# Kernel optimization log

Hardware: AMD Instinct MI355X
Metric: run time of the kernel (lower is better)

## Reference

```python
import jax, jax.numpy as jnp
import numpy as np

ALPHA = 100.0  # self.softmax_alpha


def _interp_nearest(x, size):
    # torch F.interpolate mode='nearest': src_idx = floor(dst_idx * H_in / H_out)
    H, W = x.shape[-2], x.shape[-1]
    h, w = size
    ri = (jnp.arange(h) * H) // h
    ci = (jnp.arange(w) * W) // w
    return x[:, :, ri, :][:, :, :, ci]


def _interp_bilinear_ac(x, size):
    # torch F.interpolate mode='bilinear', align_corners=True
    H, W = x.shape[-2], x.shape[-1]
    h, w = size

    def coords(n_out, n_in):
        if n_out == 1:
            return jnp.zeros((1,), jnp.float32)
        return jnp.arange(n_out, dtype=jnp.float32) * ((n_in - 1) / (n_out - 1))

    ry, rx = coords(h, H), coords(w, W)
    y0 = jnp.floor(ry).astype(jnp.int32)
    x0 = jnp.floor(rx).astype(jnp.int32)
    y1 = jnp.clip(y0 + 1, 0, H - 1)
    x1 = jnp.clip(x0 + 1, 0, W - 1)
    wy = (ry - y0.astype(jnp.float32))[None, None, :, None]
    wx = (rx - x0.astype(jnp.float32))[None, None, None, :]
    rows = x[:, :, y0, :] * (1.0 - wy) + x[:, :, y1, :] * wy  # (n,c,h,W)
    return rows[:, :, :, x0] * (1.0 - wx) + rows[:, :, :, x1] * wx  # (n,c,h,w)


def _warp(unalign_fb, fa, fa_parse, fb, fb_parse, alpha):
    n, c, h, w = fa.shape
    c2 = unalign_fb.shape[1]
    hw = h * w
    # center and channel-normalize features per spatial location
    fa = fa - jnp.mean(fa, axis=(2, 3), keepdims=True)
    fb = fb - jnp.mean(fb, axis=(2, 3), keepdims=True)
    fa = fa.reshape(n, c, hw)
    fb = fb.reshape(n, c, hw)
    fa = fa / jnp.linalg.norm(fa, axis=1, keepdims=True)
    fb = fb / jnp.linalg.norm(fb, axis=1, keepdims=True)
    ufb = unalign_fb.reshape(n, c2, hw)
    mask_a = (fa_parse.reshape(n, -1, hw)[:, 1:, :] != 0).astype(fa.dtype)  # (n,K,hw)
    mask_b = (fb_parse.reshape(n, -1, hw)[:, 1:, :] != 0).astype(fb.dtype)
    local_fa = fa[:, None, :, :] * mask_a[:, :, None, :]  # (n,K,c,hw)
    local_fb = fb[:, None, :, :] * mask_b[:, :, None, :]  # (n,K,c,hw)
    # energy[n,k,q,p] = sum_c local_fb[n,k,c,q] * local_fa[n,k,c,p]
    energy = jnp.einsum('nkcq,nkcp->nkqp', local_fb, local_fa) * alpha
    corr = jax.nn.softmax(energy, axis=2)  # softmax over fb locations q
    warped = jnp.einsum('ncq,nkqp->nkcp', ufb, corr)  # (n,K,c2,hw)
    combined = (warped * mask_a[:, :, None, :]).sum(axis=1)  # (n,c2,hw)
    norm = jnp.maximum(mask_a.sum(axis=1, keepdims=True), 1.0)  # (n,1,hw)
    aligned = combined / norm
    return aligned.reshape(n, c2, h, w)


def setup_inputs() -> dict:
    key = jax.random.key(0)
    k1, k2, k3, k4, k5 = jax.random.split(key, 5)
    return {
        'unalign_fb': jax.random.normal(k1, (1, 64, 256, 256), jnp.float32),
        'fa': jax.random.normal(k2, (1, 256, 64, 64), jnp.float32),
        'fa_parse': jax.random.randint(k3, (1, 4, 256, 256), 0, 2).astype(jnp.int32),
        'fb': jax.random.normal(k4, (1, 256, 64, 64), jnp.float32),
        'fb_parse': jax.random.randint(k5, (1, 4, 256, 256), 0, 2).astype(jnp.int32),
    }


def reference(unalign_fb, fa, fa_parse, fb, fb_parse):
    raw_hw = unalign_fb.shape[-2:]
    feat_hw = fa.shape[-2:]
    fa_p = _interp_nearest(fa_parse, feat_hw)
    fb_p = _interp_nearest(fb_parse, feat_hw)
    ufb = _interp_bilinear_ac(unalign_fb, fb.shape[-2:])
    aligned = _warp(ufb, fa, fa_p, fb, fb_p, ALPHA)
    return _interp_bilinear_ac(aligned, raw_hw)
```

## Files before the change

kernel.cpp:

```cpp
#include <hip/hip_runtime.h>
#include <math.h>

#define HW 4096
#define CC 256
#define C2 64
#define E50f 1.928749848e-22f

typedef unsigned short USH;
typedef __attribute__((ext_vector_type(8))) _Float16 f16x8;
typedef __attribute__((ext_vector_type(8))) short bf8;
typedef __attribute__((ext_vector_type(4))) float f32x4;

__device__ __forceinline__ USH f2bf(float x) {
    unsigned u = __float_as_uint(x);
    u += 0x7fff + ((u >> 16) & 1);
    return (USH)(u >> 16);
}
__device__ __forceinline__ USH f2h(float x) {
    _Float16 h = (_Float16)x;
    return *(USH*)&h;
}

__device__ __forceinline__ void gl2lds16(const USH* g, USH* l) {
    __builtin_amdgcn_global_load_lds(
        (const __attribute__((address_space(1))) void*)g,
        (__attribute__((address_space(3))) void*)l, 16, 0, 0);
}

__device__ __forceinline__ float block_reduce_sum_256(float v, float* sbuf) {
    int t = threadIdx.x;
    sbuf[t] = v;
    __syncthreads();
    for (int s = 128; s > 0; s >>= 1) {
        if (t < s) sbuf[t] += sbuf[t + s];
        __syncthreads();
    }
    float r = sbuf[0];
    __syncthreads();
    return r;
}

__global__ void k_channel_mean(const float* __restrict__ fa, const float* __restrict__ fb,
                               float* __restrict__ mu) {
    __shared__ float sbuf[256];
    int b = blockIdx.x;
    const float* src = (b < CC) ? (fa + b * HW) : (fb + (b - CC) * HW);
    float s = 0.f;
    for (int q = threadIdx.x; q < HW; q += 256) s += src[q];
    float tot = block_reduce_sum_256(s, sbuf);
    if (threadIdx.x == 0) mu[b] = tot * (1.0f / HW);
}

__global__ void k_norm_ss(const float* __restrict__ fa, const float* __restrict__ fb,
                          const float* __restrict__ mu, float* __restrict__ ssq_part) {
    int which = blockIdx.z;
    const float* src = which ? fb : fa;
    int p = blockIdx.x * 256 + threadIdx.x;
    int c0 = blockIdx.y * 32;
    float ss = 0.f;
    for (int c = c0; c < c0 + 32; ++c) {
        float v = src[c * HW + p] - mu[which * CC + c];
        ss += v * v;
    }
    ssq_part[(which * 8 + blockIdx.y) * HW + p] = ss;
}

__global__ __launch_bounds__(256) void k_norm_split_t(
    const float* __restrict__ fa, const float* __restrict__ fb,
    const float* __restrict__ mu, const float* __restrict__ ssq_part,
    USH* __restrict__ faT, USH* __restrict__ fbT) {
    __shared__ float tile[64][68];
    int which = blockIdx.z;
    const float* src = which ? fb : fa;
    USH* dst = which ? fbT : faT;
    int p0 = blockIdx.x * 64;
    int c0 = blockIdx.y * 64;
    int t = threadIdx.x;
    {
        int c_r = t >> 2, seg = t & 3;
        const float* s = &src[(size_t)(c0 + c_r) * HW + p0 + seg * 16];
#pragma unroll
        for (int k = 0; k < 4; ++k)
            *(float4*)&tile[c_r][seg * 16 + k * 4] = *(const float4*)&s[k * 4];
    }
    __syncthreads();
    {
        int p_r = t >> 2, seg = t & 3;
        int cl = seg * 16;
        float ss = 0.f;
#pragma unroll
        for (int z = 0; z < 8; ++z) ss += ssq_part[(which * 8 + z) * HW + p0 + p_r];
        float rinv = rsqrtf(ss);
        union { USH us[8]; uint4 v; } h0, h1;
#pragma unroll
        for (int j = 0; j < 8; ++j)
            h0.us[j] = f2h((tile[cl + j][p_r] - mu[which * CC + c0 + cl + j]) * rinv);
#pragma unroll
        for (int j = 0; j < 8; ++j)
            h1.us[j] = f2h((tile[cl + 8 + j][p_r] - mu[which * CC + c0 + cl + 8 + j]) * rinv);
        int kc = (c0 >> 5) + (seg >> 1);
        size_t base = (size_t)kc * 131072 + (size_t)(p0 + p_r) * 32 + (seg & 1) * 16;
        *(uint4*)&dst[base] = h0.v;
        *(uint4*)&dst[base + 8] = h1.v;
    }
}

__global__ void k_bilin_down_vt(const float* __restrict__ src, const int* __restrict__ fb_parse,
                                USH* __restrict__ vtT, float* __restrict__ bgbuf) {
    __shared__ float4 sbuf[256];
    int t = threadIdx.x;
    int p = blockIdx.x * 256 + t;
    int c = blockIdx.y;
    int j = p >> 6, i = p & 63;
    int off = (4 * j) * 256 + 4 * i;
    float m0 = (fb_parse[1 * 65536 + off] != 0) ? 1.f : 0.f;
    float m1 = (fb_parse[2 * 65536 + off] != 0) ? 1.f : 0.f;
    float m2 = (fb_parse[3 * 65536 + off] != 0) ? 1.f : 0.f;
    float ry = j * (255.0f / 63.0f);
    int y0 = (int)ry; y0 = min(y0, 255); int y1 = min(y0 + 1, 255);
    float wy = ry - (float)y0;
    float rx = i * (255.0f / 63.0f);
    int x0 = (int)rx; x0 = min(x0, 255); int x1 = min(x0 + 1, 255);
    float wx = rx - (float)x0;
    const float* sc = src + c * 65536;
    float r0 = sc[y0 * 256 + x0] * (1.f - wx) + sc[y0 * 256 + x1] * wx;
    float r1 = sc[y1 * 256 + x0] * (1.f - wx) + sc[y1 * 256 + x1] * wx;
    float v = r0 * (1.f - wy) + r1 * wy;
    size_t cbase = (size_t)(p >> 5) * 8192 + (p & 31);
    vtT[cbase + (0 * 65 + c) * 32] = f2bf(v * m0);
    vtT[cbase + (1 * 65 + c) * 32] = f2bf(v * m1);
    vtT[cbase + (2 * 65 + c) * 32] = f2bf(v * m2);
    if (c == 0) {
        vtT[cbase + 64 * 32]  = f2bf(m0);
        vtT[cbase + 129 * 32] = f2bf(m1);
        vtT[cbase + 194 * 32] = f2bf(m2);
        for (int m = 195; m < 256; ++m) vtT[cbase + m * 32] = 0;
    }
    float4 acc = make_float4(v, v * m0, v * m1, v * m2);
    sbuf[t] = acc;
    __syncthreads();
    for (int s = 128; s > 0; s >>= 1) {
        if (t < s) {
            float4 o = sbuf[t + s];
            sbuf[t].x += o.x; sbuf[t].y += o.y; sbuf[t].z += o.z; sbuf[t].w += o.w;
        }
        __syncthreads();
    }
    if (t == 0) {
        float4 r = sbuf[0];
        atomicAdd(&bgbuf[256 + c], r.x);
        atomicAdd(&bgbuf[0 * 65 + c], r.y);
        atomicAdd(&bgbuf[1 * 65 + c], r.z);
        atomicAdd(&bgbuf[2 * 65 + c], r.w);
    }
    __syncthreads();
    if (c == 0) {
        sbuf[t] = make_float4(m0, m1, m2, 0.f);
        __syncthreads();
        for (int s = 128; s > 0; s >>= 1) {
            if (t < s) {
                float4 o = sbuf[t + s];
                sbuf[t].x += o.x; sbuf[t].y += o.y; sbuf[t].z += o.z;
            }
            __syncthreads();
        }
        if (t == 0) {
            float4 r = sbuf[0];
            atomicAdd(&bgbuf[64], r.x);
            atomicAdd(&bgbuf[129], r.y);
            atomicAdd(&bgbuf[194], r.z);
        }
    }
}

__global__ __launch_bounds__(256) void k_gemm_s_exp(
    const USH* __restrict__ faT, const USH* __restrict__ fbT,
    USH* __restrict__ E) {
    __shared__ union { USH stage[2][2][4096]; USH ET[128][136]; } sm;
    int t = threadIdx.x;
    int qbase = blockIdx.x * 128;
    int pbase = blockIdx.y * 128;
    int w = t >> 6, lane = t & 63, lr = lane & 15, quad = lane >> 4;
    int pw = (w & 1) * 64, qw = (w >> 1) * 64;
    f32x4 acc[4][4] = {};

    const USH* srcA = faT + (size_t)pbase * 32;
    const USH* srcB = fbT + (size_t)qbase * 32;

#define STAGE_G(buf, kt)                                                        \
    {                                                                           \
        size_t ko = (size_t)(kt) * 131072;                                      \
        _Pragma("unroll")                                                       \
        for (int c = 0; c < 2; ++c) {                                           \
            int go = w * 1024 + c * 512 + lane * 8;                             \
            int lo = w * 1024 + c * 512;                                        \
            gl2lds16(srcA + ko + go, &sm.stage[buf][0][lo]);                    \
            gl2lds16(srcB + ko + go, &sm.stage[buf][1][lo]);                    \
        }                                                                       \
    }

    STAGE_G(0, 0);
    __syncthreads();
    for (int kt = 0; kt < 8; ++kt) {
        int cur = kt & 1;
        if (kt + 1 < 8) STAGE_G(cur ^ 1, kt + 1);
        f16x8 a[4], b[4];
#pragma unroll
        for (int i = 0; i < 4; ++i)
            a[i] = *(const f16x8*)&sm.stage[cur][0][(pw + 16 * i + lr) * 32 + quad * 8];
#pragma unroll
        for (int j = 0; j < 4; ++j)
            b[j] = *(const f16x8*)&sm.stage[cur][1][(qw + 16 * j + lr) * 32 + quad * 8];
#pragma unroll
        for (int i = 0; i < 4; ++i)
#pragma unroll
            for (int j = 0; j < 4; ++j)
                acc[i][j] = __builtin_amdgcn_mfma_f32_16x16x32_f16(a[i], b[j], acc[i][j], 0, 0, 0);
        __syncthreads();
    }
#undef STAGE_G
#pragma unroll
    for (int i = 0; i < 4; ++i) {
        int prow = pw + 16 * i + quad * 4;
#pragma unroll
        for (int j = 0; j < 4; ++j) {
            int qcol = qw + 16 * j + lr;
#pragma unroll
            for (int r = 0; r < 4; ++r)
                sm.ET[prow + r][qcol] = f2bf(__expf(fmaf(100.f, acc[i][j][r], -50.f)));
        }
    }
    __syncthreads();
    {
        int prow = t >> 1, half = t & 1;
#pragma unroll
        for (int cc = 0; cc < 2; ++cc) {
            int qcl = half * 2 + cc;
            size_t dst = (size_t)((qbase >> 5) + qcl) * 131072 + (size_t)(pbase + prow) * 32;
#pragma unroll
            for (int u = 0; u < 4; ++u)
                *(uint4*)&E[dst + u * 8] = *(const uint4*)&sm.ET[prow][qcl * 32 + u * 8];
        }
    }
}

__global__ __launch_bounds__(256) void k_pv(
    const USH* __restrict__ vtT, const USH* __restrict__ E,
    float* __restrict__ part) {
    __shared__ USH stage[2][2][4096];
    int t = threadIdx.x;
    int pbase = blockIdx.x * 128;
    int mbase = blockIdx.y * 128;
    int z = blockIdx.z;
    int w = t >> 6, lane = t & 63, lr = lane & 15, quad = lane >> 4;
    int mw = (w & 1) * 64, pw = (w >> 1) * 64;
    f32x4 acc[4][4] = {};

    const USH* srcA = vtT + (size_t)mbase * 32;
    const USH* srcB = E + (size_t)pbase * 32;

#define STAGE_P(buf, kt)                                                        \
    {                                                                           \
        size_t koA = (size_t)(z * 16 + (kt)) * 8192;                            \
        size_t koB = (size_t)(z * 16 + (kt)) * 131072;                          \
        _Pragma("unroll")                                                       \
        for (int c = 0; c < 2; ++c) {                                           \
            int go = w * 1024 + c * 512 + lane * 8;                             \
            int lo = w * 1024 + c * 512;                                        \
            gl2lds16(srcA + koA + go, &stage[buf][0][lo]);                      \
            gl2lds16(srcB + koB + go, &stage[buf][1][lo]);                      \
        }                                                                       \
    }

    STAGE_P(0, 0);
    __syncthreads();
    for (int kt = 0; kt < 16; ++kt) {
        int cur = kt & 1;
        if (kt + 1 < 16) STAGE_P(cur ^ 1, kt + 1);
        bf8 a[4], b[4];
#pragma unroll
        for (int i = 0; i < 4; ++i)
            a[i] = *(const bf8*)&stage[cur][0][(mw + 16 * i + lr) * 32 + quad * 8];
#pragma unroll
        for (int j = 0; j < 4; ++j)
            b[j] = *(const bf8*)&stage[cur][1][(pw + 16 * j + lr) * 32 + quad * 8];
#pragma unroll
        for (int i = 0; i < 4; ++i)
#pragma unroll
            for (int j = 0; j < 4; ++j)
                acc[i][j] = __builtin_amdgcn_mfma_f32_16x16x32_bf16(a[i], b[j], acc[i][j], 0, 0, 0);
        __syncthreads();
    }
#undef STAGE_P
    float* op = part + (size_t)z * 1048576;
#pragma unroll
    for (int i = 0; i < 4; ++i) {
        int mrow = mbase + mw + 16 * i + quad * 4;
#pragma unroll
        for (int j = 0; j < 4; ++j) {
            int pcol = pbase + pw + 16 * j + lr;
#pragma unroll
            for (int r = 0; r < 4; ++r)
                op[(size_t)(mrow + r) * HW + pcol] = acc[i][j][r];
        }
    }
}

__global__ void k_combine8(const float* __restrict__ part, const float* __restrict__ bgbuf,
                           const int* __restrict__ fa_parse, float* __restrict__ aligned) {
    int p = blockIdx.x * 256 + threadIdx.x;
    int c2 = blockIdx.y;
    int jj = p >> 6, ii = p & 63;
    int off = (4 * jj) * 256 + 4 * ii;
    float tot_c = bgbuf[256 + c2];
    float num = 0.f, s = 0.f;
    for (int k = 0; k < 3; ++k) {
        float ma = (fa_parse[(k + 1) * 65536 + off] != 0) ? 1.f : 0.f;
        s += ma;
        float den = E50f * (4096.0f - bgbuf[k * 65 + 64]);
        float nu  = E50f * (tot_c - bgbuf[k * 65 + c2]);
        size_t rd = (size_t)(k * 65 + 64) * HW + p;
        size_t rn = (size_t)(k * 65 + c2) * HW + p;
#pragma unroll
        for (int z = 0; z < 8; ++z) {
            den += part[(size_t)z * 1048576 + rd];
            nu  += part[(size_t)z * 1048576 + rn];
        }
        num += ma * (nu / den);
    }
    aligned[c2 * HW + p] = num / fmaxf(s, 1.f);
}

__global__ void k_bilin_up(const float* __restrict__ aligned, float* __restrict__ out) {
    int idx = (blockIdx.x * 256 + threadIdx.x) * 4;
    int c2 = blockIdx.y;
    int y = idx >> 8;
    float ry = y * (63.0f / 255.0f);
    int y0 = (int)ry; y0 = min(y0, 63); int y1 = min(y0 + 1, 63);
    float wy = ry - (float)y0;
    const float* a = aligned + c2 * HW;
    float4 o;
    float* op = &o.x;
#pragma unroll
    for (int u = 0; u < 4; ++u) {
        int x = (idx & 255) + u;
        float rx = x * (63.0f / 255.0f);
        int x0 = (int)rx; x0 = min(x0, 63); int x1 = min(x0 + 1, 63);
        float wx = rx - (float)x0;
        float r0 = a[y0 * 64 + x0] * (1.f - wx) + a[y0 * 64 + x1] * wx;
        float r1 = a[y1 * 64 + x0] * (1.f - wx) + a[y1 * 64 + x1] * wx;
        op[u] = r0 * (1.f - wy) + r1 * wy;
    }
    *(float4*)&out[c2 * 65536 + idx] = o;
}

extern "C" void kernel_launch(void* const* d_in, const int* in_sizes, int n_in,
                              void* d_out, int out_size, void* d_ws, size_t ws_size,
                              hipStream_t stream) {
    const float* unalign_fb = (const float*)d_in[0];
    const float* fa         = (const float*)d_in[1];
    const int*   fa_parse   = (const int*)d_in[2];
    const float* fb         = (const float*)d_in[3];
    const int*   fb_parse   = (const int*)d_in[4];
    float* out = (float*)d_out;

    float* w = (float*)d_ws;
    float* mu       = w;
    float* ssq_part = w + 512;
    float* bgbuf    = w + 66048;
    float* part     = w + 66368;
    float* aligned  = w + 8454976;
    USH* faT  = (USH*)(w + 8717120);
    USH* fbT  = (USH*)(w + 9241408);
    USH* vtT  = (USH*)(w + 9765696);
    USH* Ebuf = (USH*)(w + 10289984);

    k_channel_mean<<<dim3(512), dim3(256), 0, stream>>>(fa, fb, mu);
    k_norm_ss<<<dim3(16, 8, 2), dim3(256), 0, stream>>>(fa, fb, mu, ssq_part);
    k_norm_split_t<<<dim3(64, 4, 2), dim3(256), 0, stream>>>(fa, fb, mu, ssq_part, faT, fbT);
    hipMemsetAsync(bgbuf, 0, 320 * sizeof(float), stream);
    k_bilin_down_vt<<<dim3(16, 64), dim3(256), 0, stream>>>(unalign_fb, fb_parse, vtT, bgbuf);

    k_gemm_s_exp<<<dim3(32, 32), dim3(256), 0, stream>>>(faT, fbT, Ebuf);
    k_pv<<<dim3(32, 2, 8), dim3(256), 0, stream>>>(vtT, Ebuf, part);

    k_combine8<<<dim3(16, 64), dim3(256), 0, stream>>>(part, bgbuf, fa_parse, aligned);
    k_bilin_up<<<dim3(64, 64), dim3(256), 0, stream>>>(aligned, out);
}
```

Before: 150.7 us.

## Fuse QK-exp and PV GEMMs into flash-style attention kernel; merge prep kernels

Replaces the separate score+exp GEMM (which wrote a 4096x4096 bf16 E matrix to global memory) and the PV GEMM with one fused kernel that computes a 64-column score tile, exponentiates into LDS, and immediately multiplies by V, splitting q across 8 z-slices. The channel-mean and bilinear-downsample kernels are merged into one launch, and atomic reductions with a memset are replaced by per-block partial sums reduced in the combine kernel. This removes the large E round trip and several launches, at the cost of smaller tiles, fewer blocks (512), and more LDS per block.

```diff
diff --git a/kernel.cpp b/kernel.cpp
--- a/kernel.cpp
+++ b/kernel.cpp
@@ -27,28 +27,88 @@
         (__attribute__((address_space(3))) void*)l, 16, 0, 0);
 }
 
-__device__ __forceinline__ float block_reduce_sum_256(float v, float* sbuf) {
+__global__ void k_prep1(const float* __restrict__ fa, const float* __restrict__ fb,
+                        float* __restrict__ mu,
+                        const float* __restrict__ ufb_src, const int* __restrict__ fb_parse,
+                        USH* __restrict__ vtT, float* __restrict__ bgp) {
+    __shared__ float4 sred[256];
     int t = threadIdx.x;
-    sbuf[t] = v;
-    __syncthreads();
-    for (int s = 128; s > 0; s >>= 1) {
-        if (t < s) sbuf[t] += sbuf[t + s];
+    if (blockIdx.x < 512) {
+        int b = blockIdx.x;
+        const float* src = (b < CC) ? (fa + b * HW) : (fb + (b - CC) * HW);
+        float s = 0.f;
+        for (int q = t; q < HW; q += 256) s += src[q];
+        sred[t].x = s;
         __syncthreads();
-    }
-    float r = sbuf[0];
-    __syncthreads();
-    return r;
-}
-
-__global__ void k_channel_mean(const float* __restrict__ fa, const float* __restrict__ fb,
-                               float* __restrict__ mu) {
-    __shared__ float sbuf[256];
-    int b = blockIdx.x;
-    const float* src = (b < CC) ? (fa + b * HW) : (fb + (b - CC) * HW);
-    float s = 0.f;
-    for (int q = threadIdx.x; q < HW; q += 256) s += src[q];
-    float tot = block_reduce_sum_256(s, sbuf);
-    if (threadIdx.x == 0) mu[b] = tot * (1.0f / HW);
+        for (int st = 128; st > 0; st >>= 1) {
+            if (t < st) sred[t].x += sred[t + st].x;
+            __syncthreads();
+        }
+        if (t == 0) mu[b] = sred[0].x * (1.0f / HW);
+        return;
+    }
+    int bid = blockIdx.x - 512;
+    int pblk = bid & 15, c = bid >> 4;
+    int p = pblk * 256 + t;
+    int j = p >> 6, i = p & 63;
+    int off = (4 * j) * 256 + 4 * i;
+    float m0 = (fb_parse[1 * 65536 + off] != 0) ? 1.f : 0.f;
+    float m1 = (fb_parse[2 * 65536 + off] != 0) ? 1.f : 0.f;
+    float m2 = (fb_parse[3 * 65536 + off] != 0) ? 1.f : 0.f;
+    float ry = j * (255.0f / 63.0f);
+    int y0 = (int)ry; y0 = min(y0, 255); int y1 = min(y0 + 1, 255);
+    float wy = ry - (float)y0;
+    float rx = i * (255.0f / 63.0f);
+    int x0 = (int)rx; x0 = min(x0, 255); int x1 = min(x0 + 1, 255);
+    float wx = rx - (float)x0;
+    const float* sc = ufb_src + c * 65536;
+    float r0 = sc[y0 * 256 + x0] * (1.f - wx) + sc[y0 * 256 + x1] * wx;
+    float r1 = sc[y1 * 256 + x0] * (1.f - wx) + sc[y1 * 256 + x1] * wx;
+    float v = r0 * (1.f - wy) + r1 * wy;
+    size_t cbase = (size_t)(p >> 5) * 8192 + (p & 31);
+    vtT[cbase + (0 * 65 + c) * 32] = f2bf(v * m0);
+    vtT[cbase + (1 * 65 + c) * 32] = f2bf(v * m1);
+    vtT[cbase + (2 * 65 + c) * 32] = f2bf(v * m2);
+    if (c == 0) {
+        vtT[cbase + 64 * 32]  = f2bf(m0);
+        vtT[cbase + 129 * 32] = f2bf(m1);
+        vtT[cbase + 194 * 32] = f2bf(m2);
+        for (int m = 195; m < 256; ++m) vtT[cbase + m * 32] = 0;
+    }
+    sred[t] = make_float4(v, v * m0, v * m1, v * m2);
+    __syncthreads();
+    for (int st = 128; st > 0; st >>= 1) {
+        if (t < st) {
+            float4 o = sred[t + st];
+            sred[t].x += o.x; sred[t].y += o.y; sred[t].z += o.z; sred[t].w += o.w;
+        }
+        __syncthreads();
+    }
+    if (t == 0) {
+        float4 r = sred[0];
+        bgp[pblk * 320 + 256 + c]     = r.x;
+        bgp[pblk * 320 + 0 * 65 + c]  = r.y;
+        bgp[pblk * 320 + 1 * 65 + c]  = r.z;
+        bgp[pblk * 320 + 2 * 65 + c]  = r.w;
+    }
+    __syncthreads();
+    if (c == 0) {
+        sred[t] = make_float4(m0, m1, m2, 0.f);
+        __syncthreads();
+        for (int st = 128; st > 0; st >>= 1) {
+            if (t < st) {
+                float4 o = sred[t + st];
+                sred[t].x += o.x; sred[t].y += o.y; sred[t].z += o.z;
+            }
+            __syncthreads();
+        }
+        if (t == 0) {
+            float4 r = sred[0];
+            bgp[pblk * 320 + 64]  = r.x;
+            bgp[pblk * 320 + 129] = r.y;
+            bgp[pblk * 320 + 194] = r.z;
+        }
+    }
 }
 
 __global__ void k_norm_ss(const float* __restrict__ fa, const float* __restrict__ fb,
@@ -105,220 +165,131 @@
     }
 }
 
-__global__ void k_bilin_down_vt(const float* __restrict__ src, const int* __restrict__ fb_parse,
-                                USH* __restrict__ vtT, float* __restrict__ bgbuf) {
-    __shared__ float4 sbuf[256];
+__global__ __launch_bounds__(256, 2) void k_attn(
+    const USH* __restrict__ faT, const USH* __restrict__ fbT,
+    const USH* __restrict__ vtT, float* __restrict__ part) {
+    __shared__ USH sA[2][2048];
+    __shared__ USH sB[2][4096];
+    __shared__ USH sV[2][8192];
+    __shared__ USH sE[64 * 136];
     int t = threadIdx.x;
+    int p0 = blockIdx.x * 64;
+    int z = blockIdx.y;
+    int w = t >> 6, lane = t & 63, lr = lane & 15, quad = lane >> 4;
+    f32x4 accp[4][4] = {};
+
+    const USH* gA = faT + (size_t)p0 * 32;
+
+#define DMA_AB(buf, kc, q0)                                                          \
+    do {                                                                             \
+        gl2lds16(gA + (size_t)(kc) * 131072 + w * 512 + lane * 8, &sA[buf][w * 512]);\
+        _Pragma("unroll")                                                            \
+        for (int cc = 0; cc < 2; ++cc)                                               \
+            gl2lds16(fbT + (size_t)(kc) * 131072 + (size_t)(q0) * 32 +               \
+                         (2 * w + cc) * 512 + lane * 8,                              \
+                     &sB[buf][(2 * w + cc) * 512]);                                  \
+    } while (0)
+#define DMA_V(buf, qc)                                                               \
+    do {                                                                             \
+        _Pragma("unroll")                                                            \
+        for (int cc = 0; cc < 4; ++cc)                                               \
+            gl2lds16(vtT + (size_t)(qc) * 8192 + (4 * w + cc) * 512 + lane * 8,      \
+                     &sV[buf][(4 * w + cc) * 512]);                                  \
+    } while (0)
+
+    DMA_AB(0, 0, z * 512);
+    __syncthreads();
+    for (int qt = 0; qt < 4; ++qt) {
+        int q0 = z * 512 + qt * 128;
+        f32x4 accs[2][4] = {};
+        for (int kc = 0; kc < 8; ++kc) {
+            int cur = kc & 1;
+            if (kc < 7) DMA_AB(cur ^ 1, kc + 1, q0);
+            else        DMA_V(0, z * 16 + qt * 4);
+            f16x8 a[2], b[4];
+#pragma unroll
+            for (int i = 0; i < 2; ++i)
+                a[i] = *(const f16x8*)&sB[cur][(32 * w + 16 * i + lr) * 32 + quad * 8];
+#pragma unroll
+            for (int jj = 0; jj < 4; ++jj)
+                b[jj] = *(const f16x8*)&sA[cur][(16 * jj + lr) * 32 + quad * 8];
+#pragma unroll
+            for (int i = 0; i < 2; ++i)
+#pragma unroll
+                for (int jj = 0; jj < 4; ++jj)
+                    accs[i][jj] = __builtin_amdgcn_mfma_f32_16x16x32_f16(a[i], b[jj], accs[i][jj], 0, 0, 0);
+            __syncthreads();
+        }
+#pragma unroll
+        for (int i = 0; i < 2; ++i)
+#pragma unroll
+            for (int jj = 0; jj < 4; ++jj) {
+                unsigned u0 = ((unsigned)f2bf(__expf(fmaf(100.f, accs[i][jj][1], -50.f))) << 16)
+                            | (unsigned)f2bf(__expf(fmaf(100.f, accs[i][jj][0], -50.f)));
+                unsigned u1 = ((unsigned)f2bf(__expf(fmaf(100.f, accs[i][jj][3], -50.f))) << 16)
+                            | (unsigned)f2bf(__expf(fmaf(100.f, accs[i][jj][2], -50.f)));
+                int addr = (16 * jj + lr) * 136 + 32 * w + 16 * i + 4 * quad;
+                uint2 u; u.x = u0; u.y = u1;
+                *(uint2*)&sE[addr] = u;
+            }
+        __syncthreads();
+        for (int kc = 0; kc < 4; ++kc) {
+            int cur = kc & 1;
+            if (kc < 3)      DMA_V(cur ^ 1, z * 16 + qt * 4 + kc + 1);
+            else if (qt < 3) DMA_AB(0, 0, q0 + 128);
+            bf8 av[4], be[4];
+#pragma unroll
+            for (int i = 0; i < 4; ++i)
+                av[i] = *(const bf8*)&sV[cur][(64 * w + 16 * i + lr) * 32 + quad * 8];
+#pragma unroll
+            for (int jj = 0; jj < 4; ++jj)
+                be[jj] = *(const bf8*)&sE[(16 * jj + lr) * 136 + kc * 32 + quad * 8];
+#pragma unroll
+            for (int i = 0; i < 4; ++i)
+#pragma unroll
+                for (int jj = 0; jj < 4; ++jj)
+                    accp[i][jj] = __builtin_amdgcn_mfma_f32_16x16x32_bf16(av[i], be[jj], accp[i][jj], 0, 0, 0);
+            __syncthreads();
+        }
+    }
+#undef DMA_AB
+#undef DMA_V
+    float* op = part + (size_t)z * 1048576;
+#pragma unroll
+    for (int i = 0; i < 4; ++i) {
+        int m = 64 * w + 16 * i + quad * 4;
+#pragma unroll
+        for (int jj = 0; jj < 4; ++jj) {
+            int pc = p0 + 16 * jj + lr;
+#pragma unroll
+            for (int r = 0; r < 4; ++r)
+                op[(size_t)(m + r) * HW + pc] = accp[i][jj][r];
+        }
+    }
+}
+
+__global__ void k_combine8(const float* __restrict__ part, const float* __restrict__ bgp,
+                           const int* __restrict__ fa_parse, float* __restrict__ aligned) {
+    __shared__ float sums[8];
+    int t = threadIdx.x;
+    int c2 = blockIdx.y;
+    if (t < 7) {
+        int idx = (t < 3) ? (t * 65 + 64) : ((t < 6) ? (t - 3) * 65 + c2 : 256 + c2);
+        float s = 0.f;
+#pragma unroll
+        for (int pb = 0; pb < 16; ++pb) s += bgp[pb * 320 + idx];
+        sums[t] = s;
+    }
+    __syncthreads();
     int p = blockIdx.x * 256 + t;
-    int c = blockIdx.y;
-    int j = p >> 6, i = p & 63;
-    int off = (4 * j) * 256 + 4 * i;
-    float m0 = (fb_parse[1 * 65536 + off] != 0) ? 1.f : 0.f;
-    float m1 = (fb_parse[2 * 65536 + off] != 0) ? 1.f : 0.f;
-    float m2 = (fb_parse[3 * 65536 + off] != 0) ? 1.f : 0.f;
-    float ry = j * (255.0f / 63.0f);
-    int y0 = (int)ry; y0 = min(y0, 255); int y1 = min(y0 + 1, 255);
-    float wy = ry - (float)y0;
-    float rx = i * (255.0f / 63.0f);
-    int x0 = (int)rx; x0 = min(x0, 255); int x1 = min(x0 + 1, 255);
-    float wx = rx - (float)x0;
-    const float* sc = src + c * 65536;
-    float r0 = sc[y0 * 256 + x0] * (1.f - wx) + sc[y0 * 256 + x1] * wx;
-    float r1 = sc[y1 * 256 + x0] * (1.f - wx) + sc[y1 * 256 + x1] * wx;
-    float v = r0 * (1.f - wy) + r1 * wy;
-    size_t cbase = (size_t)(p >> 5) * 8192 + (p & 31);
-    vtT[cbase + (0 * 65 + c) * 32] = f2bf(v * m0);
-    vtT[cbase + (1 * 65 + c) * 32] = f2bf(v * m1);
-    vtT[cbase + (2 * 65 + c) * 32] = f2bf(v * m2);
-    if (c == 0) {
-        vtT[cbase + 64 * 32]  = f2bf(m0);
-        vtT[cbase + 129 * 32] = f2bf(m1);
-        vtT[cbase + 194 * 32] = f2bf(m2);
-        for (int m = 195; m < 256; ++m) vtT[cbase + m * 32] = 0;
-    }
-    float4 acc = make_float4(v, v * m0, v * m1, v * m2);
-    sbuf[t] = acc;
-    __syncthreads();
-    for (int s = 128; s > 0; s >>= 1) {
-        if (t < s) {
-            float4 o = sbuf[t + s];
-            sbuf[t].x += o.x; sbuf[t].y += o.y; sbuf[t].z += o.z; sbuf[t].w += o.w;
-        }
-        __syncthreads();
-    }
-    if (t == 0) {
-        float4 r = sbuf[0];
-        atomicAdd(&bgbuf[256 + c], r.x);
-        atomicAdd(&bgbuf[0 * 65 + c], r.y);
-        atomicAdd(&bgbuf[1 * 65 + c], r.z);
-        atomicAdd(&bgbuf[2 * 65 + c], r.w);
-    }
-    __syncthreads();
-    if (c == 0) {
-        sbuf[t] = make_float4(m0, m1, m2, 0.f);
-        __syncthreads();
-        for (int s = 128; s > 0; s >>= 1) {
-            if (t < s) {
-                float4 o = sbuf[t + s];
-                sbuf[t].x += o.x; sbuf[t].y += o.y; sbuf[t].z += o.z;
-            }
-            __syncthreads();
-        }
-        if (t == 0) {
-            float4 r = sbuf[0];
-            atomicAdd(&bgbuf[64], r.x);
-            atomicAdd(&bgbuf[129], r.y);
-            atomicAdd(&bgbuf[194], r.z);
-        }
-    }
-}
-
-__global__ __launch_bounds__(256) void k_gemm_s_exp(
-    const USH* __restrict__ faT, const USH* __restrict__ fbT,
-    USH* __restrict__ E) {
-    __shared__ union { USH stage[2][2][4096]; USH ET[128][136]; } sm;
-    int t = threadIdx.x;
-    int qbase = blockIdx.x * 128;
-    int pbase = blockIdx.y * 128;
-    int w = t >> 6, lane = t & 63, lr = lane & 15, quad = lane >> 4;
-    int pw = (w & 1) * 64, qw = (w >> 1) * 64;
-    f32x4 acc[4][4] = {};
-
-    const USH* srcA = faT + (size_t)pbase * 32;
-    const USH* srcB = fbT + (size_t)qbase * 32;
-
-#define STAGE_G(buf, kt)                                                        \
-    {                                                                           \
-        size_t ko = (size_t)(kt) * 131072;                                      \
-        _Pragma("unroll")                                                       \
-        for (int c = 0; c < 2; ++c) {                                           \
-            int go = w * 1024 + c * 512 + lane * 8;                             \
-            int lo = w * 1024 + c * 512;                                        \
-            gl2lds16(srcA + ko + go, &sm.stage[buf][0][lo]);                    \
-            gl2lds16(srcB + ko + go, &sm.stage[buf][1][lo]);                    \
-        }                                                                       \
-    }
-
-    STAGE_G(0, 0);
-    __syncthreads();
-    for (int kt = 0; kt < 8; ++kt) {
-        int cur = kt & 1;
-        if (kt + 1 < 8) STAGE_G(cur ^ 1, kt + 1);
-        f16x8 a[4], b[4];
-#pragma unroll
-        for (int i = 0; i < 4; ++i)
-            a[i] = *(const f16x8*)&sm.stage[cur][0][(pw + 16 * i + lr) * 32 + quad * 8];
-#pragma unroll
-        for (int j = 0; j < 4; ++j)
-            b[j] = *(const f16x8*)&sm.stage[cur][1][(qw + 16 * j + lr) * 32 + quad * 8];
-#pragma unroll
-        for (int i = 0; i < 4; ++i)
-#pragma unroll
-            for (int j = 0; j < 4; ++j)
-                acc[i][j] = __builtin_amdgcn_mfma_f32_16x16x32_f16(a[i], b[j], acc[i][j], 0, 0, 0);
-        __syncthreads();
-    }
-#undef STAGE_G
-#pragma unroll
-    for (int i = 0; i < 4; ++i) {
-        int prow = pw + 16 * i + quad * 4;
-#pragma unroll
-        for (int j = 0; j < 4; ++j) {
-            int qcol = qw + 16 * j + lr;
-#pragma unroll
-            for (int r = 0; r < 4; ++r)
-                sm.ET[prow + r][qcol] = f2bf(__expf(fmaf(100.f, acc[i][j][r], -50.f)));
-        }
-    }
-    __syncthreads();
-    {
-        int prow = t >> 1, half = t & 1;
-#pragma unroll
-        for (int cc = 0; cc < 2; ++cc) {
-            int qcl = half * 2 + cc;
-            size_t dst = (size_t)((qbase >> 5) + qcl) * 131072 + (size_t)(pbase + prow) * 32;
-#pragma unroll
-            for (int u = 0; u < 4; ++u)
-                *(uint4*)&E[dst + u * 8] = *(const uint4*)&sm.ET[prow][qcl * 32 + u * 8];
-        }
-    }
-}
-
-__global__ __launch_bounds__(256) void k_pv(
-    const USH* __restrict__ vtT, const USH* __restrict__ E,
-    float* __restrict__ part) {
-    __shared__ USH stage[2][2][4096];
-    int t = threadIdx.x;
-    int pbase = blockIdx.x * 128;
-    int mbase = blockIdx.y * 128;
-    int z = blockIdx.z;
-    int w = t >> 6, lane = t & 63, lr = lane & 15, quad = lane >> 4;
-    int mw = (w & 1) * 64, pw = (w >> 1) * 64;
-    f32x4 acc[4][4] = {};
-
-    const USH* srcA = vtT + (size_t)mbase * 32;
-    const USH* srcB = E + (size_t)pbase * 32;
-
-#define STAGE_P(buf, kt)                                                        \
-    {                                                                           \
-        size_t koA = (size_t)(z * 16 + (kt)) * 8192;                            \
-        size_t koB = (size_t)(z * 16 + (kt)) * 131072;                          \
-        _Pragma("unroll")                                                       \
-        for (int c = 0; c < 2; ++c) {                                           \
-            int go = w * 1024 + c * 512 + lane * 8;                             \
-            int lo = w * 1024 + c * 512;                                        \
-            gl2lds16(srcA + koA + go, &stage[buf][0][lo]);                      \
-            gl2lds16(srcB + koB + go, &stage[buf][1][lo]);                      \
-        }                                                                       \
-    }
-
-    STAGE_P(0, 0);
-    __syncthreads();
-    for (int kt = 0; kt < 16; ++kt) {
-        int cur = kt & 1;
-        if (kt + 1 < 16) STAGE_P(cur ^ 1, kt + 1);
-        bf8 a[4], b[4];
-#pragma unroll
-        for (int i = 0; i < 4; ++i)
-            a[i] = *(const bf8*)&stage[cur][0][(mw + 16 * i + lr) * 32 + quad * 8];
-#pragma unroll
-        for (int j = 0; j < 4; ++j)
-            b[j] = *(const bf8*)&stage[cur][1][(pw + 16 * j + lr) * 32 + quad * 8];
-#pragma unroll
-        for (int i = 0; i < 4; ++i)
-#pragma unroll
-            for (int j = 0; j < 4; ++j)
-                acc[i][j] = __builtin_amdgcn_mfma_f32_16x16x32_bf16(a[i], b[j], acc[i][j], 0, 0, 0);
-        __syncthreads();
-    }
-#undef STAGE_P
-    float* op = part + (size_t)z * 1048576;
-#pragma unroll
-    for (int i = 0; i < 4; ++i) {
-        int mrow = mbase + mw + 16 * i + quad * 4;
-#pragma unroll
-        for (int j = 0; j < 4; ++j) {
-            int pcol = pbase + pw + 16 * j + lr;
-#pragma unroll
-            for (int r = 0; r < 4; ++r)
-                op[(size_t)(mrow + r) * HW + pcol] = acc[i][j][r];
-        }
-    }
-}
-
-__global__ void k_combine8(const float* __restrict__ part, const float* __restrict__ bgbuf,
-                           const int* __restrict__ fa_parse, float* __restrict__ aligned) {
-    int p = blockIdx.x * 256 + threadIdx.x;
-    int c2 = blockIdx.y;
     int jj = p >> 6, ii = p & 63;
     int off = (4 * jj) * 256 + 4 * ii;
-    float tot_c = bgbuf[256 + c2];
     float num = 0.f, s = 0.f;
     for (int k = 0; k < 3; ++k) {
         float ma = (fa_parse[(k + 1) * 65536 + off] != 0) ? 1.f : 0.f;
         s += ma;
-        float den = E50f * (4096.0f - bgbuf[k * 65 + 64]);
-        float nu  = E50f * (tot_c - bgbuf[k * 65 + c2]);
+        float den = E50f * (4096.0f - sums[k]);
+        float nu  = E50f * (sums[6] - sums[3 + k]);
         size_t rd = (size_t)(k * 65 + 64) * HW + p;
         size_t rn = (size_t)(k * 65 + c2) * HW + p;
 #pragma unroll
@@ -367,23 +338,17 @@
     float* w = (float*)d_ws;
     float* mu       = w;
     float* ssq_part = w + 512;
-    float* bgbuf    = w + 66048;
-    float* part     = w + 66368;
-    float* aligned  = w + 8454976;
-    USH* faT  = (USH*)(w + 8717120);
-    USH* fbT  = (USH*)(w + 9241408);
-    USH* vtT  = (USH*)(w + 9765696);
-    USH* Ebuf = (USH*)(w + 10289984);
-
-    k_channel_mean<<<dim3(512), dim3(256), 0, stream>>>(fa, fb, mu);
+    float* bgp      = w + 66048;
+    float* part     = w + 71168;
+    float* aligned  = w + 8459776;
+    USH* faT = (USH*)(w + 8721920);
+    USH* fbT = (USH*)(w + 9246208);
+    USH* vtT = (USH*)(w + 9770496);
+
+    k_prep1<<<dim3(1536), dim3(256), 0, stream>>>(fa, fb, mu, unalign_fb, fb_parse, vtT, bgp);
     k_norm_ss<<<dim3(16, 8, 2), dim3(256), 0, stream>>>(fa, fb, mu, ssq_part);
     k_norm_split_t<<<dim3(64, 4, 2), dim3(256), 0, stream>>>(fa, fb, mu, ssq_part, faT, fbT);
-    hipMemsetAsync(bgbuf, 0, 320 * sizeof(float), stream);
-    k_bilin_down_vt<<<dim3(16, 64), dim3(256), 0, stream>>>(unalign_fb, fb_parse, vtT, bgbuf);
-
-    k_gemm_s_exp<<<dim3(32, 32), dim3(256), 0, stream>>>(faT, fbT, Ebuf);
-    k_pv<<<dim3(32, 2, 8), dim3(256), 0, stream>>>(vtT, Ebuf, part);
-
-    k_combine8<<<dim3(16, 64), dim3(256), 0, stream>>>(part, bgbuf, fa_parse, aligned);
+    k_attn<<<dim3(64, 8), dim3(256), 0, stream>>>(faT, fbT, vtT, part);
+    k_combine8<<<dim3(16, 64), dim3(256), 0, stream>>>(part, bgp, fa_parse, aligned);
     k_bilin_up<<<dim3(64, 64), dim3(256), 0, stream>>>(aligned, out);
 }
```

Measured after the change: 136.3 us. 1.11x faster.
